# Kernel optimization log

Hardware: AMD Instinct MI355X
Metric: run time of the kernel (lower is better)

Reference implementation:

```python
import jax, jax.numpy as jnp
import numpy as np
from jax import lax

B, T, F, E, H = 512, 256, 256, 256, 256


def setup_inputs() -> dict:
    key = jax.random.key(0)
    ks = jax.random.split(key, 13)
    s = 0.05  # small param scale for numerical sanity
    return {
        "features": jax.random.normal(ks[0], (B, T, F), jnp.float32),
        "molecule_lengths": jax.random.randint(ks[1], (B,), 1, T + 1, jnp.int32),
        "W_embed": jax.random.normal(ks[2], (E, F), jnp.float32) * s,
        "W_ih": jax.random.normal(ks[3], (4 * H, E + H + F), jnp.float32) * s,
        "b_ih": jax.random.normal(ks[4], (4 * H,), jnp.float32) * s,
        "W_hh": jax.random.normal(ks[5], (4 * H, H), jnp.float32) * s,
        "b_hh": jax.random.normal(ks[6], (4 * H,), jnp.float32) * s,
        "W_att": jax.random.normal(ks[7], (E, H), jnp.float32) * s,
        "W_final": jax.random.normal(ks[8], (1, H), jnp.float32) * s,
        "b_final": jax.random.normal(ks[9], (1,), jnp.float32) * s,
        "q0": jax.random.normal(ks[10], (B, H), jnp.float32),
        "c0": jax.random.normal(ks[11], (B, H), jnp.float32),
        "r0": jax.random.normal(ks[12], (B, E), jnp.float32),
    }


def reference(features, molecule_lengths, W_embed, W_ih, b_ih, W_hh, b_hh,
              W_att, W_final, b_final, q0, c0, r0):
    # pad_mask[b,t] True where atom t is padding (t >= length)
    pad_mask = jnp.arange(T)[None, :] >= molecule_lengths[:, None]  # [B,T]
    embedding = jnp.einsum('btf,ef->bte', features, W_embed)        # [B,T,E]

    def step(carry, x_t):
        q, c, r = carry
        q_star = jnp.concatenate([q, r, x_t], axis=1)  # [B, E+H+F]
        gates = q_star @ W_ih.T + b_ih + q @ W_hh.T + b_hh  # [B,4H]
        i_g, f_g, g_g, o_g = jnp.split(gates, 4, axis=1)    # torch gate order
        c = jax.nn.sigmoid(f_g) * c + jax.nn.sigmoid(i_g) * jnp.tanh(g_g)
        q = jax.nn.sigmoid(o_g) * jnp.tanh(c)
        # masked attention over atoms
        qp = q @ W_att.T                                  # [B,E]
        e = jnp.einsum('bte,be->bt', embedding, qp)       # [B,T]
        e = jnp.where(pad_mask, -jnp.inf, e)
        alpha = jax.nn.softmax(e, axis=1)                 # [B,T]
        r = jnp.einsum('bte,bt->be', embedding, alpha)    # [B,E]
        return (q, c, r), q

    _, dec = lax.scan(step, (q0, c0, r0), jnp.swapaxes(features, 0, 1))
    dec = jnp.swapaxes(dec, 0, 1)                         # [B,T,H]
    out = jax.nn.relu(dec) @ W_final.T + b_final          # [B,T,1] (dropout = eval mode)
    out = out[..., 0]
    return jnp.where(pad_mask, 0.0, out)                  # [B,T]
```

## Files before the change

kernel.cpp:

```cpp
#include <hip/hip_runtime.h>
#include <hip/hip_bf16.h>

#define B_   512
#define T_   256
#define F_   256
#define E_   256
#define H_   256
#define G4_  1024
#define K_   768
#define NT   1024
#define NBLK 256

typedef __attribute__((ext_vector_type(8))) short short8;
typedef __attribute__((ext_vector_type(8))) unsigned short ushort8v;
typedef __attribute__((ext_vector_type(4))) unsigned short ushort4v;
typedef __attribute__((ext_vector_type(4))) float f32x4;

__device__ __forceinline__ float bf2f(unsigned int u) {
  union { unsigned int i; float f; } v; v.i = u << 16; return v.f;
}
__device__ __forceinline__ unsigned short f2bf(float f) {
  union { __hip_bfloat16 h; unsigned short u; } v;
  v.h = __float2bfloat16(f); return v.u;
}
__device__ __forceinline__ float sigm(float x) { return 1.f / (1.f + __expf(-x)); }
__device__ __forceinline__ float tanh_fast(float x) { return 1.f - 2.f / (1.f + __expf(2.f * x)); }

__global__ void setup_pack(const float* __restrict__ W_ih, const float* __restrict__ W_hh,
                           const float* __restrict__ b_ih, const float* __restrict__ b_hh,
                           const float* __restrict__ W_att, const float* __restrict__ W_embed,
                           unsigned short* __restrict__ Bg, unsigned short* __restrict__ Bx,
                           unsigned short* __restrict__ Ba, unsigned short* __restrict__ We,
                           float* __restrict__ bcomb) {
  int idx = blockIdx.x * blockDim.x + threadIdx.x;
  if (idx < G4_ * K_) {
    int o = idx, j = o & 7, lane = (o >> 3) & 63, rem = o >> 9;
    int kt = rem % 24, ntw = rem / 24;
    int n = ntw * 16 + (lane & 15);
    int k = kt * 32 + ((lane >> 4) << 3) + j;
    float v = W_ih[n * K_ + k] + (k < H_ ? W_hh[n * H_ + k] : 0.f);
    Bg[o] = f2bf(v);
    return;
  }
  idx -= G4_ * K_;
  if (idx < G4_ * F_) {
    int o = idx, j = o & 7, lane = (o >> 3) & 63, rem = o >> 9;
    int kt = rem & 7, ntw = rem >> 3;
    int n = ntw * 16 + (lane & 15);
    int k = kt * 32 + ((lane >> 4) << 3) + j;
    Bx[o] = f2bf(W_ih[n * K_ + 512 + k]);
    return;
  }
  idx -= G4_ * F_;
  if (idx < E_ * H_) {
    int o = idx, j = o & 7, lane = (o >> 3) & 63, rem = o >> 9;
    int kt = rem & 7, ntw = rem >> 3;
    int n = ntw * 16 + (lane & 15), k = kt * 32 + ((lane >> 4) << 3) + j;
    Ba[o] = f2bf(W_att[n * H_ + k]);
    return;
  }
  idx -= E_ * H_;
  if (idx < E_ * F_) {
    int o = idx, j = o & 7, lane = (o >> 3) & 63, rem = o >> 9;
    int kt = rem & 7, ntw = rem >> 3;
    int n = ntw * 16 + (lane & 15), k = kt * 32 + ((lane >> 4) << 3) + j;
    We[o] = f2bf(W_embed[n * F_ + k]);
    return;
  }
  idx -= E_ * F_;
  if (idx < G4_) bcomb[idx] = b_ih[idx] + b_hh[idx];
}

__global__ void sort_kernel(const int* __restrict__ lengths, int* __restrict__ perm) {
  __shared__ int lens[B_];
  int tid = threadIdx.x;
  lens[tid] = lengths[tid];
  __syncthreads();
  int L = lens[tid], pos = 0;
  for (int i = 0; i < B_; ++i) {
    int li = lens[i];
    pos += (li < L) || (li == L && i < tid);
  }
  perm[pos] = tid;
}

__global__ __launch_bounds__(256)
void gx_kernel(const float* __restrict__ features, const unsigned short* __restrict__ Bx,
               unsigned short* __restrict__ gxw) {
  __shared__ unsigned short featL[T_][264];
  const int b = blockIdx.x;
  const int tid = threadIdx.x, w = tid >> 6, lane = tid & 63;
  const float* fb = features + (size_t)b * T_ * F_;
  for (int c4 = 0; c4 < 64; ++c4) {
    float4 v = *reinterpret_cast<const float4*>(fb + (size_t)tid * F_ + c4 * 4);
    featL[tid][c4 * 4 + 0] = f2bf(v.x);
    featL[tid][c4 * 4 + 1] = f2bf(v.y);
    featL[tid][c4 * 4 + 2] = f2bf(v.z);
    featL[tid][c4 * 4 + 3] = f2bf(v.w);
  }
  __syncthreads();
  const short8* BX = reinterpret_cast<const short8*>(Bx);
  for (int nt = w; nt < 64; nt += 4) {
    short8 Bf[8];
    #pragma unroll
    for (int kt = 0; kt < 8; ++kt) Bf[kt] = BX[(nt * 8 + kt) * 64 + lane];
    for (int mt = 0; mt < 16; ++mt) {
      f32x4 acc = f32x4{0.f, 0.f, 0.f, 0.f};
      #pragma unroll
      for (int kt = 0; kt < 8; ++kt) {
        short8 a = *reinterpret_cast<const short8*>(
            &featL[mt * 16 + (lane & 15)][kt * 32 + ((lane >> 4) << 3)]);
        acc = __builtin_amdgcn_mfma_f32_16x16x32_bf16(a, Bf[kt], acc, 0, 0, 0);
      }
      #pragma unroll
      for (int reg = 0; reg < 4; ++reg) {
        int t = mt * 16 + (lane >> 4) * 4 + reg;
        gxw[((size_t)b * T_ + t) * G4_ + nt * 16 + (lane & 15)] = f2bf(acc[reg]);
      }
    }
  }
}

template <int USE_GX>
__global__ __launch_bounds__(NT)
void mol_kernel(const float* __restrict__ features, const int* __restrict__ lengths,
                const int* __restrict__ perm,
                const unsigned short* __restrict__ Bg, const unsigned short* __restrict__ Ba,
                const unsigned short* __restrict__ We, const float* __restrict__ bcomb,
                const float* __restrict__ Wfin, const float* __restrict__ bfin,
                const float* __restrict__ q0, const float* __restrict__ c0,
                const float* __restrict__ r0, const unsigned short* __restrict__ gxw,
                float* __restrict__ out) {
  __shared__ __align__(16) unsigned short emb[T_][264];
  __shared__ __align__(16) unsigned short qs[784];
  __shared__ __align__(16) unsigned short qpb[272];
  __shared__ float gates[G4_];
  __shared__ float esc[T_];
  __shared__ float rpart[16][264];
  __shared__ float redf[16];

  const int tid  = threadIdx.x;
  const int w    = tid >> 6;
  const int lane = tid & 63;
  const int l15  = lane & 15;
  const float bfinal = bfin[0];
  const int KTL = USE_GX ? 16 : 24;

  float wfr = 0.f, bc0 = 0.f, bc1 = 0.f, bc2 = 0.f, bc3 = 0.f;
  if (tid < H_) {
    wfr = Wfin[tid];
    bc0 = bcomb[tid]; bc1 = bcomb[H_ + tid];
    bc2 = bcomb[2 * H_ + tid]; bc3 = bcomb[3 * H_ + tid];
  }

  const short8* BW  = reinterpret_cast<const short8*>(Bg);
  const short8* BA  = reinterpret_cast<const short8*>(Ba);
  const short8* WE  = reinterpret_cast<const short8*>(We);
  const short8* qs8 = reinterpret_cast<const short8*>(qs);

  short8 barf[8];
  #pragma unroll
  for (int kt = 0; kt < 8; ++kt) barf[kt] = BA[(w * 8 + kt) * 64 + lane];

  for (int half = 0; half < 2; ++half) {
    const int b   = perm[half == 0 ? (int)blockIdx.x : (B_ - 1 - (int)blockIdx.x)];
    const int len = lengths[b];
    const float* featb = features + (size_t)b * T_ * F_;
    const unsigned short* gxb = USE_GX ? (gxw + (size_t)b * T_ * G4_) : nullptr;
    const int nmt = (len + 15) >> 4;

    float cstr = 0.f;
    if (tid < H_) {
      cstr = c0[(size_t)b * H_ + tid];
      qs[tid]       = f2bf(q0[(size_t)b * H_ + tid]);
      qs[H_ + tid]  = f2bf(r0[(size_t)b * E_ + tid]);
      esc[tid] = -3.0e38f;
      if (!USE_GX) qs[512 + tid] = f2bf(featb[tid]);
    }

    for (int mt = 0; mt < nmt; ++mt) {
      f32x4 ea = f32x4{0.f, 0.f, 0.f, 0.f};
      #pragma unroll
      for (int kt = 0; kt < 8; ++kt) {
        const float* ap_ = featb + (size_t)(mt * 16 + l15) * F_ + kt * 32 + ((lane >> 4) << 3);
        float4 fa = *reinterpret_cast<const float4*>(ap_);
        float4 fb4 = *reinterpret_cast<const float4*>(ap_ + 4);
        short8 a;
        a[0] = (short)f2bf(fa.x);  a[1] = (short)f2bf(fa.y);
        a[2] = (short)f2bf(fa.z);  a[3] = (short)f2bf(fa.w);
        a[4] = (short)f2bf(fb4.x); a[5] = (short)f2bf(fb4.y);
        a[6] = (short)f2bf(fb4.z); a[7] = (short)f2bf(fb4.w);
        ea = __builtin_amdgcn_mfma_f32_16x16x32_bf16(a, WE[(w * 8 + kt) * 64 + lane], ea, 0, 0, 0);
      }
      #pragma unroll
      for (int reg = 0; reg < 4; ++reg) {
        int t = mt * 16 + (lane >> 4) * 4 + reg;
        emb[t][w * 16 + l15] = f2bf(ea[reg]);
      }
    }

    for (int t = 0; t < len; ++t) {
      __syncthreads();

      unsigned short gxu0 = 0, gxu1 = 0, gxu2 = 0, gxu3 = 0;
      float xnext = 0.f;
      if (USE_GX) {
        if (tid < H_) {
          const unsigned short* gp = gxb + (size_t)t * G4_ + tid;
          gxu0 = gp[0]; gxu1 = gp[256]; gxu2 = gp[512]; gxu3 = gp[768];
        }
      } else {
        if (tid < H_ && t + 1 < T_) xnext = featb[(size_t)(t + 1) * F_ + tid];
      }

      {
        f32x4 acc[4];
        #pragma unroll
        for (int nt = 0; nt < 4; ++nt) acc[nt] = f32x4{0.f, 0.f, 0.f, 0.f};
        short8 cur[4], nxt[4];
        #pragma unroll
        for (int nt = 0; nt < 4; ++nt) cur[nt] = BW[((w * 4 + nt) * 24 + 0) * 64 + lane];
        for (int kt = 0; kt < KTL; ++kt) {
          if (kt + 1 < KTL) {
            #pragma unroll
            for (int nt = 0; nt < 4; ++nt) nxt[nt] = BW[((w * 4 + nt) * 24 + kt + 1) * 64 + lane];
          }
          short8 a = qs8[kt * 4 + (lane >> 4)];
          #pragma unroll
          for (int nt = 0; nt < 4; ++nt)
            acc[nt] = __builtin_amdgcn_mfma_f32_16x16x32_bf16(a, cur[nt], acc[nt], 0, 0, 0);
          #pragma unroll
          for (int nt = 0; nt < 4; ++nt) cur[nt] = nxt[nt];
        }
        if (lane < 16) {
          #pragma unroll
          for (int nt = 0; nt < 4; ++nt) gates[w * 64 + nt * 16 + lane] = acc[nt][0];
        }
      }
      __syncthreads();

      if (tid < H_) {
        float ig = gates[tid]           + bc0;
        float fg = gates[H_ + tid]      + bc1;
        float gg = gates[2 * H_ + tid]  + bc2;
        float og = gates[3 * H_ + tid]  + bc3;
        if (USE_GX) {
          ig += bf2f(gxu0); fg += bf2f(gxu1); gg += bf2f(gxu2); og += bf2f(gxu3);
        }
        float cn = sigm(fg) * cstr + sigm(ig) * tanh_fast(gg);
        float qn = sigm(og) * tanh_fast(cn);
        cstr = cn;
        qs[tid] = f2bf(qn);
        float po = fmaxf(qn, 0.f) * wfr;
        #pragma unroll
        for (int s = 32; s >= 1; s >>= 1) po += __shfl_xor(po, s);
        if (lane == 0) redf[w] = po;
      } else if (lane == 0) {
        redf[w] = 0.f;
      }
      __syncthreads();

      if (tid == 0) {
        float s = 0.f;
        #pragma unroll
        for (int i = 0; i < 16; ++i) s += redf[i];
        out[(size_t)b * T_ + t] = s + bfinal;
      }
      {
        f32x4 a0 = f32x4{0.f, 0.f, 0.f, 0.f};
        #pragma unroll
        for (int kt = 0; kt < 8; ++kt) {
          short8 a = qs8[kt * 4 + (lane >> 4)];
          a0 = __builtin_amdgcn_mfma_f32_16x16x32_bf16(a, barf[kt], a0, 0, 0, 0);
        }
        if (lane < 16) qpb[w * 16 + lane] = f2bf(a0[0]);
      }
      __syncthreads();

      {
        const int mt = w;
        if (mt < nmt) {
          f32x4 acc = f32x4{0.f, 0.f, 0.f, 0.f};
          #pragma unroll
          for (int kt = 0; kt < 8; ++kt) {
            short8 a  = *reinterpret_cast<const short8*>(
                &emb[mt * 16 + l15][kt * 32 + ((lane >> 4) << 3)]);
            short8 bq = *reinterpret_cast<const short8*>(
                &qpb[kt * 32 + ((lane >> 4) << 3)]);
            acc = __builtin_amdgcn_mfma_f32_16x16x32_bf16(a, bq, acc, 0, 0, 0);
          }
          if (l15 == 0) {
            #pragma unroll
            for (int reg = 0; reg < 4; ++reg) {
              int tt = mt * 16 + (lane >> 4) * 4 + reg;
              esc[tt] = (tt < len) ? acc[reg] : -3.0e38f;
            }
          }
        }
      }
      __syncthreads();

      float rinv, p0, p1, p2, p3;
      {
        float v0 = esc[lane], v1 = esc[lane + 64], v2 = esc[lane + 128], v3 = esc[lane + 192];
        float m = fmaxf(fmaxf(v0, v1), fmaxf(v2, v3));
        #pragma unroll
        for (int s = 32; s >= 1; s >>= 1) m = fmaxf(m, __shfl_xor(m, s));
        p0 = __expf(v0 - m); p1 = __expf(v1 - m); p2 = __expf(v2 - m); p3 = __expf(v3 - m);
        float sv = p0 + p1 + p2 + p3;
        #pragma unroll
        for (int s = 32; s >= 1; s >>= 1) sv += __shfl_xor(sv, s);
        rinv = 1.f / sv;
      }

      {
        const int t0 = w * 16;
        const int tmax = (t0 + 16 < len) ? (t0 + 16) : len;
        const int sbase = (w & 3) * 16;
        const int ksel = w >> 2;
        float vsel = (ksel == 0) ? p0 : (ksel == 1) ? p1 : (ksel == 2) ? p2 : p3;
        float r0a = 0.f, r1a = 0.f, r2a = 0.f, r3a = 0.f;
        for (int i = 0; t0 + i < tmax; ++i) {
          float p = __shfl(vsel, sbase + i);
          ushort4v ev = *reinterpret_cast<const ushort4v*>(&emb[t0 + i][lane * 4]);
          r0a += p * bf2f(ev[0]); r1a += p * bf2f(ev[1]);
          r2a += p * bf2f(ev[2]); r3a += p * bf2f(ev[3]);
        }
        f32x4 rv = {r0a, r1a, r2a, r3a};
        *reinterpret_cast<f32x4*>(&rpart[w][lane * 4]) = rv;
      }
      __syncthreads();

      if (tid < H_) {
        float s = 0.f;
        #pragma unroll
        for (int sl = 0; sl < 16; ++sl) s += rpart[sl][tid];
        qs[H_ + tid] = f2bf(s * rinv);
        if (!USE_GX) qs[512 + tid] = f2bf(xnext);
      }
    }

    for (int tt = len + tid; tt < T_; tt += NT) out[(size_t)b * T_ + tt] = 0.f;
    __syncthreads();
  }
}

extern "C" void kernel_launch(void* const* d_in, const int* in_sizes, int n_in,
                              void* d_out, int out_size, void* d_ws, size_t ws_size,
                              hipStream_t stream) {
  const float* features = (const float*)d_in[0];
  const int*   lengths  = (const int*)d_in[1];
  const float* W_embed  = (const float*)d_in[2];
  const float* W_ih     = (const float*)d_in[3];
  const float* b_ih     = (const float*)d_in[4];
  const float* W_hh     = (const float*)d_in[5];
  const float* b_hh     = (const float*)d_in[6];
  const float* W_att    = (const float*)d_in[7];
  const float* W_final  = (const float*)d_in[8];
  const float* b_final  = (const float*)d_in[9];
  const float* q0       = (const float*)d_in[10];
  const float* c0       = (const float*)d_in[11];
  const float* r0       = (const float*)d_in[12];
  float* out = (float*)d_out;

  char* ws = (char*)d_ws;
  unsigned short* Bg    = (unsigned short*)(ws + 0);
  unsigned short* Bx    = (unsigned short*)(ws + 1572864);
  unsigned short* Ba    = (unsigned short*)(ws + 2097152);
  unsigned short* We    = (unsigned short*)(ws + 2228224);
  float*          bcomb = (float*)(ws + 2359296);
  int*            perm  = (int*)(ws + 2363392);
  unsigned short* gxw   = (unsigned short*)(ws + 2365440);
  const size_t need_gx = 2365440ull + 268435456ull;
  const int use_gx = (ws_size >= need_gx) ? 1 : 0;

  const int setup_elems = G4_ * K_ + G4_ * F_ + E_ * H_ + E_ * F_ + G4_;
  setup_pack<<<(setup_elems + 255) / 256, 256, 0, stream>>>(
      W_ih, W_hh, b_ih, b_hh, W_att, W_embed, Bg, Bx, Ba, We, bcomb);
  sort_kernel<<<1, B_, 0, stream>>>(lengths, perm);
  if (use_gx) {
    gx_kernel<<<B_, 256, 0, stream>>>(features, Bx, gxw);
    mol_kernel<1><<<NBLK, NT, 0, stream>>>(
        features, lengths, perm, Bg, Ba, We, bcomb,
        W_final, b_final, q0, c0, r0, gxw, out);
  } else {
    mol_kernel<0><<<NBLK, NT, 0, stream>>>(
        features, lengths, perm, Bg, Ba, We, bcomb,
        W_final, b_final, q0, c0, r0, gxw, out);
  }
}
```

Baseline: 3.546 ms.

## Split LSTM gate GEMM to overlap q-part with attention scoring

Restructures the recurrent loop by peeling the first step and splitting the gate matmul into a q-dependent part, computed alongside the attention-score MFMA, and an r/x-dependent part computed after the attention readout. This shortens the serial critical path per timestep, since half the gate GEMM no longer waits on the softmax/readout. The cost is more live accumulator registers across phases and a more complex peeled loop structure.

```diff
diff --git a/kernel.cpp b/kernel.cpp
--- a/kernel.cpp
+++ b/kernel.cpp
@@ -175,7 +175,7 @@
       qs[tid]       = f2bf(q0[(size_t)b * H_ + tid]);
       qs[H_ + tid]  = f2bf(r0[(size_t)b * E_ + tid]);
       esc[tid] = -3.0e38f;
-      if (!USE_GX) qs[512 + tid] = f2bf(featb[tid]);
+      qs[512 + tid] = f2bf(featb[tid]);
     }
 
     for (int mt = 0; mt < nmt; ++mt) {
@@ -198,55 +198,41 @@
         emb[t][w * 16 + l15] = f2bf(ea[reg]);
       }
     }
-
-    for (int t = 0; t < len; ++t) {
-      __syncthreads();
-
+    __syncthreads();
+
+    {
       unsigned short gxu0 = 0, gxu1 = 0, gxu2 = 0, gxu3 = 0;
-      float xnext = 0.f;
-      if (USE_GX) {
-        if (tid < H_) {
-          const unsigned short* gp = gxb + (size_t)t * G4_ + tid;
-          gxu0 = gp[0]; gxu1 = gp[256]; gxu2 = gp[512]; gxu3 = gp[768];
-        }
-      } else {
-        if (tid < H_ && t + 1 < T_) xnext = featb[(size_t)(t + 1) * F_ + tid];
-      }
-
-      {
-        f32x4 acc[4];
-        #pragma unroll
-        for (int nt = 0; nt < 4; ++nt) acc[nt] = f32x4{0.f, 0.f, 0.f, 0.f};
-        short8 cur[4], nxt[4];
-        #pragma unroll
-        for (int nt = 0; nt < 4; ++nt) cur[nt] = BW[((w * 4 + nt) * 24 + 0) * 64 + lane];
-        for (int kt = 0; kt < KTL; ++kt) {
-          if (kt + 1 < KTL) {
-            #pragma unroll
-            for (int nt = 0; nt < 4; ++nt) nxt[nt] = BW[((w * 4 + nt) * 24 + kt + 1) * 64 + lane];
-          }
-          short8 a = qs8[kt * 4 + (lane >> 4)];
-          #pragma unroll
-          for (int nt = 0; nt < 4; ++nt)
-            acc[nt] = __builtin_amdgcn_mfma_f32_16x16x32_bf16(a, cur[nt], acc[nt], 0, 0, 0);
-          #pragma unroll
-          for (int nt = 0; nt < 4; ++nt) cur[nt] = nxt[nt];
-        }
-        if (lane < 16) {
-          #pragma unroll
-          for (int nt = 0; nt < 4; ++nt) gates[w * 64 + nt * 16 + lane] = acc[nt][0];
-        }
-      }
-      __syncthreads();
-
+      if (USE_GX && tid < H_) {
+        const unsigned short* gp = gxb + tid;
+        gxu0 = gp[0]; gxu1 = gp[256]; gxu2 = gp[512]; gxu3 = gp[768];
+      }
+      f32x4 acc[4];
+      #pragma unroll
+      for (int nt = 0; nt < 4; ++nt) acc[nt] = f32x4{0.f, 0.f, 0.f, 0.f};
+      short8 cur[4], nxt[4];
+      #pragma unroll
+      for (int nt = 0; nt < 4; ++nt) cur[nt] = BW[((w * 4 + nt) * 24 + 0) * 64 + lane];
+      for (int kt = 0; kt < KTL; ++kt) {
+        if (kt + 1 < KTL) {
+          #pragma unroll
+          for (int nt = 0; nt < 4; ++nt) nxt[nt] = BW[((w * 4 + nt) * 24 + kt + 1) * 64 + lane];
+        }
+        short8 a = qs8[kt * 4 + (lane >> 4)];
+        #pragma unroll
+        for (int nt = 0; nt < 4; ++nt)
+          acc[nt] = __builtin_amdgcn_mfma_f32_16x16x32_bf16(a, cur[nt], acc[nt], 0, 0, 0);
+        #pragma unroll
+        for (int nt = 0; nt < 4; ++nt) cur[nt] = nxt[nt];
+      }
+      if (lane < 16) {
+        #pragma unroll
+        for (int nt = 0; nt < 4; ++nt) gates[w * 64 + nt * 16 + lane] = acc[nt][0];
+      }
+      __syncthreads();
       if (tid < H_) {
-        float ig = gates[tid]           + bc0;
-        float fg = gates[H_ + tid]      + bc1;
-        float gg = gates[2 * H_ + tid]  + bc2;
-        float og = gates[3 * H_ + tid]  + bc3;
-        if (USE_GX) {
-          ig += bf2f(gxu0); fg += bf2f(gxu1); gg += bf2f(gxu2); og += bf2f(gxu3);
-        }
+        float ig = gates[tid] + bc0, fg = gates[H_ + tid] + bc1;
+        float gg = gates[2 * H_ + tid] + bc2, og = gates[3 * H_ + tid] + bc3;
+        if (USE_GX) { ig += bf2f(gxu0); fg += bf2f(gxu1); gg += bf2f(gxu2); og += bf2f(gxu3); }
         float cn = sigm(fg) * cstr + sigm(ig) * tanh_fast(gg);
         float qn = sigm(og) * tanh_fast(cn);
         cstr = cn;
@@ -258,71 +244,98 @@
       } else if (lane == 0) {
         redf[w] = 0.f;
       }
+    }
+
+    for (int i = 0; i < len - 1; ++i) {
       __syncthreads();
 
       if (tid == 0) {
         float s = 0.f;
         #pragma unroll
-        for (int i = 0; i < 16; ++i) s += redf[i];
-        out[(size_t)b * T_ + t] = s + bfinal;
+        for (int k2 = 0; k2 < 16; ++k2) s += redf[k2];
+        out[(size_t)b * T_ + i] = s + bfinal;
+      }
+      unsigned short gxu0 = 0, gxu1 = 0, gxu2 = 0, gxu3 = 0;
+      if (USE_GX) {
+        if (tid < H_) {
+          const unsigned short* gp = gxb + (size_t)(i + 1) * G4_ + tid;
+          gxu0 = gp[0]; gxu1 = gp[256]; gxu2 = gp[512]; gxu3 = gp[768];
+        }
+      } else {
+        if (tid < H_) qs[512 + tid] = f2bf(featb[(size_t)(i + 1) * F_ + tid]);
       }
       {
-        f32x4 a0 = f32x4{0.f, 0.f, 0.f, 0.f};
+        f32x4 aq = f32x4{0.f, 0.f, 0.f, 0.f};
         #pragma unroll
         for (int kt = 0; kt < 8; ++kt) {
           short8 a = qs8[kt * 4 + (lane >> 4)];
-          a0 = __builtin_amdgcn_mfma_f32_16x16x32_bf16(a, barf[kt], a0, 0, 0, 0);
-        }
-        if (lane < 16) qpb[w * 16 + lane] = f2bf(a0[0]);
-      }
-      __syncthreads();
-
+          aq = __builtin_amdgcn_mfma_f32_16x16x32_bf16(a, barf[kt], aq, 0, 0, 0);
+        }
+        if (lane < 16) qpb[w * 16 + lane] = f2bf(aq[0]);
+      }
+      __syncthreads();
+
+      f32x4 acc[4];
       {
-        const int mt = w;
-        if (mt < nmt) {
-          f32x4 acc = f32x4{0.f, 0.f, 0.f, 0.f};
+        #pragma unroll
+        for (int nt = 0; nt < 4; ++nt) acc[nt] = f32x4{0.f, 0.f, 0.f, 0.f};
+        short8 cur[4], nxt[4];
+        #pragma unroll
+        for (int nt = 0; nt < 4; ++nt) cur[nt] = BW[((w * 4 + nt) * 24 + 0) * 64 + lane];
+        if (w < nmt) {
+          const int mt = w;
+          f32x4 sacc = f32x4{0.f, 0.f, 0.f, 0.f};
           #pragma unroll
           for (int kt = 0; kt < 8; ++kt) {
             short8 a  = *reinterpret_cast<const short8*>(
                 &emb[mt * 16 + l15][kt * 32 + ((lane >> 4) << 3)]);
             short8 bq = *reinterpret_cast<const short8*>(
                 &qpb[kt * 32 + ((lane >> 4) << 3)]);
-            acc = __builtin_amdgcn_mfma_f32_16x16x32_bf16(a, bq, acc, 0, 0, 0);
+            sacc = __builtin_amdgcn_mfma_f32_16x16x32_bf16(a, bq, sacc, 0, 0, 0);
           }
           if (l15 == 0) {
             #pragma unroll
             for (int reg = 0; reg < 4; ++reg) {
               int tt = mt * 16 + (lane >> 4) * 4 + reg;
-              esc[tt] = (tt < len) ? acc[reg] : -3.0e38f;
+              esc[tt] = (tt < len) ? sacc[reg] : -3.0e38f;
             }
           }
         }
-      }
-      __syncthreads();
-
-      float rinv, p0, p1, p2, p3;
+        for (int kt = 0; kt < 8; ++kt) {
+          if (kt + 1 < 8) {
+            #pragma unroll
+            for (int nt = 0; nt < 4; ++nt) nxt[nt] = BW[((w * 4 + nt) * 24 + kt + 1) * 64 + lane];
+          }
+          short8 a = qs8[kt * 4 + (lane >> 4)];
+          #pragma unroll
+          for (int nt = 0; nt < 4; ++nt)
+            acc[nt] = __builtin_amdgcn_mfma_f32_16x16x32_bf16(a, cur[nt], acc[nt], 0, 0, 0);
+          #pragma unroll
+          for (int nt = 0; nt < 4; ++nt) cur[nt] = nxt[nt];
+        }
+      }
+      __syncthreads();
+
+      float rinv;
       {
         float v0 = esc[lane], v1 = esc[lane + 64], v2 = esc[lane + 128], v3 = esc[lane + 192];
         float m = fmaxf(fmaxf(v0, v1), fmaxf(v2, v3));
         #pragma unroll
         for (int s = 32; s >= 1; s >>= 1) m = fmaxf(m, __shfl_xor(m, s));
-        p0 = __expf(v0 - m); p1 = __expf(v1 - m); p2 = __expf(v2 - m); p3 = __expf(v3 - m);
+        float p0 = __expf(v0 - m), p1 = __expf(v1 - m), p2 = __expf(v2 - m), p3 = __expf(v3 - m);
         float sv = p0 + p1 + p2 + p3;
         #pragma unroll
         for (int s = 32; s >= 1; s >>= 1) sv += __shfl_xor(sv, s);
         rinv = 1.f / sv;
-      }
-
-      {
         const int t0 = w * 16;
         const int tmax = (t0 + 16 < len) ? (t0 + 16) : len;
         const int sbase = (w & 3) * 16;
         const int ksel = w >> 2;
         float vsel = (ksel == 0) ? p0 : (ksel == 1) ? p1 : (ksel == 2) ? p2 : p3;
         float r0a = 0.f, r1a = 0.f, r2a = 0.f, r3a = 0.f;
-        for (int i = 0; t0 + i < tmax; ++i) {
-          float p = __shfl(vsel, sbase + i);
-          ushort4v ev = *reinterpret_cast<const ushort4v*>(&emb[t0 + i][lane * 4]);
+        for (int k2 = 0; t0 + k2 < tmax; ++k2) {
+          float p = __shfl(vsel, sbase + k2);
+          ushort4v ev = *reinterpret_cast<const ushort4v*>(&emb[t0 + k2][lane * 4]);
           r0a += p * bf2f(ev[0]); r1a += p * bf2f(ev[1]);
           r2a += p * bf2f(ev[2]); r3a += p * bf2f(ev[3]);
         }
@@ -336,8 +349,55 @@
         #pragma unroll
         for (int sl = 0; sl < 16; ++sl) s += rpart[sl][tid];
         qs[H_ + tid] = f2bf(s * rinv);
-        if (!USE_GX) qs[512 + tid] = f2bf(xnext);
-      }
+      }
+      __syncthreads();
+
+      {
+        short8 cur[4], nxt[4];
+        #pragma unroll
+        for (int nt = 0; nt < 4; ++nt) cur[nt] = BW[((w * 4 + nt) * 24 + 8) * 64 + lane];
+        for (int kt = 8; kt < KTL; ++kt) {
+          if (kt + 1 < KTL) {
+            #pragma unroll
+            for (int nt = 0; nt < 4; ++nt) nxt[nt] = BW[((w * 4 + nt) * 24 + kt + 1) * 64 + lane];
+          }
+          short8 a = qs8[kt * 4 + (lane >> 4)];
+          #pragma unroll
+          for (int nt = 0; nt < 4; ++nt)
+            acc[nt] = __builtin_amdgcn_mfma_f32_16x16x32_bf16(a, cur[nt], acc[nt], 0, 0, 0);
+          #pragma unroll
+          for (int nt = 0; nt < 4; ++nt) cur[nt] = nxt[nt];
+        }
+        if (lane < 16) {
+          #pragma unroll
+          for (int nt = 0; nt < 4; ++nt) gates[w * 64 + nt * 16 + lane] = acc[nt][0];
+        }
+      }
+      __syncthreads();
+
+      if (tid < H_) {
+        float ig = gates[tid] + bc0, fg = gates[H_ + tid] + bc1;
+        float gg = gates[2 * H_ + tid] + bc2, og = gates[3 * H_ + tid] + bc3;
+        if (USE_GX) { ig += bf2f(gxu0); fg += bf2f(gxu1); gg += bf2f(gxu2); og += bf2f(gxu3); }
+        float cn = sigm(fg) * cstr + sigm(ig) * tanh_fast(gg);
+        float qn = sigm(og) * tanh_fast(cn);
+        cstr = cn;
+        qs[tid] = f2bf(qn);
+        float po = fmaxf(qn, 0.f) * wfr;
+        #pragma unroll
+        for (int s = 32; s >= 1; s >>= 1) po += __shfl_xor(po, s);
+        if (lane == 0) redf[w] = po;
+      } else if (lane == 0) {
+        redf[w] = 0.f;
+      }
+    }
+
+    __syncthreads();
+    if (tid == 0) {
+      float s = 0.f;
+      #pragma unroll
+      for (int k2 = 0; k2 < 16; ++k2) s += redf[k2];
+      out[(size_t)b * T_ + (len - 1)] = s + bfinal;
     }
 
     for (int tt = len + tid; tt < T_; tt += NT) out[(size_t)b * T_ + tt] = 0.f;
```

Result: slower. 10.78 ms (+204.1%).
